# Kernel optimization log

Measured on AMD Instinct MI355X. Metric: run time of the kernel, lower is better.

## Reference

```python
import jax, jax.numpy as jnp
import numpy as np

N_NODES = 50000
IN_DIM = 128
HID = 2 * IN_DIM  # 256, per module: hidden_dim = input_dims * 2
FC1 = 1024
FC2 = 512
N_ACT = 64
N_EDGES = 800000
N_AGENTS = 16384


def _layernorm(h, g, b, eps=1e-5):
    mu = jnp.mean(h, axis=-1, keepdims=True)
    var = jnp.var(h, axis=-1, keepdims=True)
    return (h - mu) * jax.lax.rsqrt(var + eps) * g + b


def setup_inputs() -> dict:
    key = jax.random.key(0)
    ks = jax.random.split(key, 16)
    def u(k, shape, fan_in):
        s = 1.0 / np.sqrt(fan_in)
        return jax.random.uniform(k, shape, jnp.float32, -s, s)
    inp = {}
    inp["x"] = jax.random.normal(ks[0], (N_NODES, IN_DIM), jnp.float32)
    inp["action"] = jax.random.normal(ks[1], (N_AGENTS, N_ACT), jnp.float32)
    inp["edge_index"] = jax.random.randint(ks[2], (2, N_EDGES), 0, N_NODES, jnp.int32)
    inp["agent_idx"] = jax.random.randint(ks[3], (N_AGENTS,), 0, N_NODES, jnp.int32)
    # GCNConv params (linear no bias + separate bias)
    inp["W_gcn"] = u(ks[4], (IN_DIM, HID), IN_DIM)
    inp["b_gcn"] = jnp.zeros((HID,), jnp.float32)
    # fc1, fc2 (custom uniform init per module)
    inp["W1"] = u(ks[5], (HID, FC1), FC1)
    inp["b1"] = u(ks[6], (FC1,), FC1)
    inp["g1"] = jnp.ones((FC1,), jnp.float32)
    inp["beta1"] = jnp.zeros((FC1,), jnp.float32)
    inp["W2"] = u(ks[7], (FC1, FC2), FC2)
    inp["b2"] = u(ks[8], (FC2,), FC2)
    inp["g2"] = jnp.ones((FC2,), jnp.float32)
    inp["beta2"] = jnp.zeros((FC2,), jnp.float32)
    inp["Wa"] = u(ks[9], (N_ACT, FC2), FC2)
    inp["ba"] = u(ks[10], (FC2,), FC2)
    inp["Wq"] = jax.random.uniform(ks[11], (FC2, 1), jnp.float32, -0.003, 0.003)
    inp["bq"] = jax.random.uniform(ks[12], (1,), jnp.float32, -0.003, 0.003)
    return inp


def reference(x, action, W_gcn, b_gcn, W1, b1, g1, beta1, W2, b2, g2, beta2, Wa, ba, Wq, bq, edge_index, agent_idx):
    N = x.shape[0]
    # GCNConv: add self-loops, symmetric D^-1/2 (A+I) D^-1/2 normalization
    loops = jnp.arange(N, dtype=edge_index.dtype)
    src = jnp.concatenate([edge_index[0], loops])
    dst = jnp.concatenate([edge_index[1], loops])
    h = x @ W_gcn  # [N, HID] transform before aggregation
    deg = jax.ops.segment_sum(jnp.ones_like(dst, dtype=h.dtype), dst, num_segments=N)
    dinv = jax.lax.rsqrt(jnp.maximum(deg, 1.0))  # deg >= 1 due to self-loops
    norm = dinv[src] * dinv[dst]  # [E+N]
    agg = jax.ops.segment_sum(h[src] * norm[:, None], dst, num_segments=N) + b_gcn
    # masked gather of agent nodes, then critic MLP
    z = jax.nn.relu(agg[agent_idx])  # [A, HID]
    s = jax.nn.relu(_layernorm(z @ W1 + b1, g1, beta1))
    s = _layernorm(s @ W2 + b2, g2, beta2)
    a = action @ Wa + ba
    sa = jax.nn.relu(s + a)
    return sa @ Wq + bq  # [A, 1]
```

## Files before the change

kernel.cpp:

```cpp
#include <hip/hip_runtime.h>
#include <hip/hip_bf16.h>

typedef _Float16 f16;
typedef _Float16 __attribute__((ext_vector_type(8))) half8;
typedef _Float16 __attribute__((ext_vector_type(4))) half4;
typedef float __attribute__((ext_vector_type(4))) floatx4;

#define IN_DIM 128
#define HID    256
#define FC1    1024
#define FC2    512
#define NACT   64

__device__ __forceinline__ void transpose_tile(const float* __restrict__ in, f16* __restrict__ out,
                                               int K, int N, int bx, int by, int tid) {
    __shared__ f16 tile[32][33];
    int k0 = bx * 32, n0 = by * 32;
    int tx = tid & 31, ty = tid >> 5;
    #pragma unroll
    for (int i = 0; i < 4; ++i)
        tile[ty + i * 8][tx] = (f16)in[(size_t)(k0 + ty + i * 8) * N + n0 + tx];
    __syncthreads();
    #pragma unroll
    for (int i = 0; i < 4; ++i)
        out[(size_t)(n0 + ty + i * 8) * K + k0 + tx] = tile[tx][ty + i * 8];
}

__device__ __forceinline__ void cvt8(const float* __restrict__ in, f16* __restrict__ out, long gi) {
    float4 a = *(const float4*)&in[gi * 8];
    float4 b = *(const float4*)&in[gi * 8 + 4];
    half8 pk;
    pk[0] = (f16)a.x; pk[1] = (f16)a.y; pk[2] = (f16)a.z; pk[3] = (f16)a.w;
    pk[4] = (f16)b.x; pk[5] = (f16)b.y; pk[6] = (f16)b.z; pk[7] = (f16)b.w;
    *(half8*)&out[gi * 8] = pk;
}

__global__ __launch_bounds__(256)
void prep_kernel(const float* __restrict__ Wgcn, const float* __restrict__ W1,
                 const float* __restrict__ W2, const float* __restrict__ Wa,
                 const float* __restrict__ action, const float* __restrict__ x,
                 f16* WgcnT, f16* W1T, f16* W2T, f16* WaT, f16* act16, f16* x16,
                 int* degcnt, int* needed, int* n_needed, int N, int A) {
    int b = blockIdx.x, tid = threadIdx.x;
    if (b < 196) {
        int i = b * 256 + tid;
        if (i < N) { degcnt[i] = 0; needed[i] = 0; }
        if (b == 0 && tid == 0) *n_needed = 0;
        return;
    }
    b -= 196;
    if (b < 32)  { transpose_tile(Wgcn, WgcnT, IN_DIM, HID, b & 3, b >> 2, tid); return; }
    b -= 32;
    if (b < 256) { transpose_tile(W1, W1T, HID, FC1, b & 7, b >> 3, tid); return; }
    b -= 256;
    if (b < 512) { transpose_tile(W2, W2T, FC1, FC2, b & 31, b >> 5, tid); return; }
    b -= 512;
    if (b < 32)  { transpose_tile(Wa, WaT, NACT, FC2, b & 1, b >> 1, tid); return; }
    b -= 32;
    if (b < 512) { cvt8(action, act16, (long)b * 256 + tid); return; }
    b -= 512;
    cvt8(x, x16, (long)b * 256 + tid);
}

__global__ void markdeg_kernel(const int* __restrict__ agent_idx, const int* __restrict__ edst,
                               int* __restrict__ needed, int* __restrict__ needed_list,
                               int* __restrict__ n_needed, int* __restrict__ degcnt, int A, int E) {
    int b = blockIdx.x;
    if (b < 64) {
        int i = b * 256 + threadIdx.x;
        if (i < A) {
            int idx = agent_idx[i];
            if (atomicCAS(&needed[idx], 0, -1) == 0) {
                int p = atomicAdd(n_needed, 1);
                needed_list[p] = idx;
                needed[idx] = p + 1;
            }
        }
        return;
    }
    int e = (b - 64) * 256 + threadIdx.x;
    if (e < E) atomicAdd(&degcnt[edst[e]], 1);
}

__global__ void dss_kernel(const int* __restrict__ degcnt, const int* __restrict__ needed,
                           const int* __restrict__ agent_idx, float* __restrict__ dinv,
                           int* __restrict__ offs, int* __restrict__ partials,
                           int* __restrict__ agent_slot, int N, int A) {
    int b = blockIdx.x;
    if (b < 196) {
        __shared__ int sh[256];
        int tid = threadIdx.x;
        int i = b * 256 + tid;
        int dc = (i < N) ? degcnt[i] : 0;
        if (i < N) dinv[i] = rsqrtf((float)dc + 1.0f);
        int v = (i < N && needed[i] != 0) ? dc : 0;
        sh[tid] = v;
        __syncthreads();
        #pragma unroll
        for (int d = 1; d < 256; d <<= 1) {
            int t = (tid >= d) ? sh[tid - d] : 0;
            __syncthreads();
            sh[tid] += t;
            __syncthreads();
        }
        if (i < N) offs[i] = sh[tid] - v;
        if (tid == 255) partials[b] = sh[255];
        return;
    }
    int i = (b - 196) * 256 + threadIdx.x;
    if (i < A) agent_slot[i] = needed[agent_idx[i]] - 1;
}

__global__ void addback_kernel(int* __restrict__ offs, const int* __restrict__ partials,
                               int* __restrict__ cursor, int n, int nblk) {
    __shared__ int sh[256];
    int tid = threadIdx.x;
    int v = (tid < nblk) ? partials[tid] : 0;
    sh[tid] = v;
    __syncthreads();
    #pragma unroll
    for (int d = 1; d < 256; d <<= 1) {
        int t = (tid >= d) ? sh[tid - d] : 0;
        __syncthreads();
        sh[tid] += t;
        __syncthreads();
    }
    int base = (blockIdx.x == 0) ? 0 : sh[blockIdx.x - 1];
    int i = blockIdx.x * 256 + tid;
    if (i < n) {
        int o = offs[i] + base;
        offs[i] = o;
        cursor[i] = o;
    }
}

__global__ void fill_kernel(const int* __restrict__ src, const int* __restrict__ dst,
                            const int* __restrict__ needed, int* __restrict__ cursor,
                            int* __restrict__ srcbuf, int E) {
    int e = blockIdx.x * blockDim.x + threadIdx.x;
    if (e < E) {
        int d = dst[e];
        if (needed[d] != 0) {
            int pos = atomicAdd(&cursor[d], 1);
            srcbuf[pos] = src[e];
        }
    }
}

__global__ __launch_bounds__(256)
void gather_x_kernel(const int* __restrict__ needed_list, const int* __restrict__ n_needed,
                     const int* __restrict__ offs, const int* __restrict__ degcnt,
                     const int* __restrict__ srcbuf, const float* __restrict__ dinv,
                     const f16* __restrict__ x16, f16* __restrict__ xagg) {
    int w = (blockIdx.x * 256 + threadIdx.x) >> 6;
    int lane = threadIdx.x & 63;
    if (w >= *n_needed) return;
    int d = needed_list[w];
    float dd = dinv[d];
    int beg = offs[d], cnt = degcnt[d];
    union { unsigned u; f16 h[2]; } ld0, ld1, ld2, ld3;
    ld0.u = *(const unsigned*)&x16[(size_t)d * IN_DIM + lane * 2];
    float ax = (float)ld0.h[0] * dd * dd, ay = (float)ld0.h[1] * dd * dd;
    int j = 0;
    for (; j + 3 < cnt; j += 4) {
        int s0 = srcbuf[beg + j], s1 = srcbuf[beg + j + 1];
        int s2 = srcbuf[beg + j + 2], s3 = srcbuf[beg + j + 3];
        float n0 = dinv[s0] * dd, n1 = dinv[s1] * dd;
        float n2 = dinv[s2] * dd, n3 = dinv[s3] * dd;
        ld0.u = *(const unsigned*)&x16[(size_t)s0 * IN_DIM + lane * 2];
        ld1.u = *(const unsigned*)&x16[(size_t)s1 * IN_DIM + lane * 2];
        ld2.u = *(const unsigned*)&x16[(size_t)s2 * IN_DIM + lane * 2];
        ld3.u = *(const unsigned*)&x16[(size_t)s3 * IN_DIM + lane * 2];
        ax = fmaf((float)ld0.h[0], n0, ax); ay = fmaf((float)ld0.h[1], n0, ay);
        ax = fmaf((float)ld1.h[0], n1, ax); ay = fmaf((float)ld1.h[1], n1, ay);
        ax = fmaf((float)ld2.h[0], n2, ax); ay = fmaf((float)ld2.h[1], n2, ay);
        ax = fmaf((float)ld3.h[0], n3, ax); ay = fmaf((float)ld3.h[1], n3, ay);
    }
    for (; j < cnt; ++j) {
        int s0 = srcbuf[beg + j];
        float n0 = dinv[s0] * dd;
        ld0.u = *(const unsigned*)&x16[(size_t)s0 * IN_DIM + lane * 2];
        ax = fmaf((float)ld0.h[0], n0, ax);
        ay = fmaf((float)ld0.h[1], n0, ay);
    }
    union { f16 h[2]; unsigned u; } pk;
    pk.h[0] = (f16)ax; pk.h[1] = (f16)ay;
    *(unsigned*)&xagg[(size_t)w * IN_DIM + lane * 2] = pk.u;
}

__device__ __forceinline__ void swz_decode(int bid, int log2ny, int& bx, int& by) {
    int xcd = bid & 7;
    int pos = bid >> 3;
    bx = (pos >> log2ny) * 8 + xcd;
    by = pos & ((1 << log2ny) - 1);
}

template<bool RELU, bool LIMIT>
__device__ __forceinline__ void gemm_tile(f16* __restrict__ smA, f16* __restrict__ smB,
                                          const f16* __restrict__ A, const f16* __restrict__ BT,
                                          f16* __restrict__ C, const float* __restrict__ bias,
                                          const int* __restrict__ limit,
                                          int bx, int by, int N, int K) {
    if (LIMIT && bx * 64 >= *limit) return;
    const int tid = threadIdx.x;
    const int lane = tid & 63;
    const int wave = tid >> 6;
    const int wr = wave >> 1, wc = wave & 1;
    const long bm = (long)bx * 64, bn = (long)by * 64;

    size_t aoff[2], boff[2];
    #pragma unroll
    for (int t = 0; t < 2; ++t) {
        int ci = t * 256 + tid;
        int r = ci >> 3, s = ci & 7, ks = s ^ (r & 7);
        aoff[t] = (size_t)(bm + r) * K + ks * 8;
        boff[t] = (size_t)(bn + r) * K + ks * 8;
    }
    int aidx[2][2], bidx[2][2];
    const int kc = lane >> 4;
    #pragma unroll
    for (int kk = 0; kk < 2; ++kk) {
        #pragma unroll
        for (int i = 0; i < 2; ++i) {
            int ar = wr * 32 + i * 16 + (lane & 15);
            aidx[kk][i] = ar * 64 + ((kk * 4 + kc) ^ (ar & 7)) * 8;
            int br = wc * 32 + i * 16 + (lane & 15);
            bidx[kk][i] = br * 64 + ((kk * 4 + kc) ^ (br & 7)) * 8;
        }
    }

    const int NT = K >> 6;
    auto stage = [&](int buf, int k0) {
        #pragma unroll
        for (int t = 0; t < 2; ++t) {
            __builtin_amdgcn_global_load_lds(
                (const __attribute__((address_space(1))) void*)(A + aoff[t] + k0),
                (__attribute__((address_space(3))) void*)(&smA[buf * 4096 + (t * 256 + tid) * 8]), 16, 0, 0);
            __builtin_amdgcn_global_load_lds(
                (const __attribute__((address_space(1))) void*)(BT + boff[t] + k0),
                (__attribute__((address_space(3))) void*)(&smB[buf * 4096 + (t * 256 + tid) * 8]), 16, 0, 0);
        }
    };

    floatx4 acc[2][2] = {};
    stage(0, 0);
    asm volatile("s_waitcnt vmcnt(0)" ::: "memory");
    __builtin_amdgcn_s_barrier();
    int cur = 0;
    for (int t = 0; t < NT; ++t) {
        if (t + 1 < NT) stage(cur ^ 1, (t + 1) << 6);
        #pragma unroll
        for (int kk = 0; kk < 2; ++kk) {
            half8 af[2], bf[2];
            #pragma unroll
            for (int i = 0; i < 2; ++i) {
                af[i] = *(const half8*)&smA[cur * 4096 + aidx[kk][i]];
                bf[i] = *(const half8*)&smB[cur * 4096 + bidx[kk][i]];
            }
            #pragma unroll
            for (int mi = 0; mi < 2; ++mi)
                #pragma unroll
                for (int ni = 0; ni < 2; ++ni)
                    acc[mi][ni] = __builtin_amdgcn_mfma_f32_16x16x32_f16(af[mi], bf[ni], acc[mi][ni], 0, 0, 0);
        }
        asm volatile("s_waitcnt vmcnt(0)" ::: "memory");
        __builtin_amdgcn_s_barrier();
        cur ^= 1;
    }
    const int col0 = (int)bn + wc * 32 + (lane & 15);
    const int row0 = (int)bm + wr * 32 + (lane >> 4) * 4;
    #pragma unroll
    for (int ni = 0; ni < 2; ++ni) {
        int col = col0 + ni * 16;
        float bz = bias[col];
        #pragma unroll
        for (int mi = 0; mi < 2; ++mi) {
            #pragma unroll
            for (int q = 0; q < 4; ++q) {
                int row = row0 + mi * 16 + q;
                float v = acc[mi][ni][q] + bz;
                if (RELU) v = fmaxf(v, 0.f);
                C[(size_t)row * N + col] = (f16)v;
            }
        }
    }
}

template<bool RELU, bool LIMIT>
__global__ __launch_bounds__(256)
void gemm_f16_kernel(const f16* __restrict__ A, const f16* __restrict__ BT,
                     f16* __restrict__ C, const float* __restrict__ bias,
                     const int* __restrict__ limit, int N, int K, int log2ny) {
    __shared__ __align__(16) f16 smA[2 * 4096];
    __shared__ __align__(16) f16 smB[2 * 4096];
    int bx, by;
    swz_decode(blockIdx.x, log2ny, bx, by);
    gemm_tile<RELU, LIMIT>(smA, smB, A, BT, C, bias, limit, bx, by, N, K);
}

__global__ __launch_bounds__(256)
void gemm_dual_kernel(const f16* __restrict__ A0, const f16* __restrict__ BT0, f16* __restrict__ C0,
                      const float* __restrict__ bias0, const int* __restrict__ limit, int K0,
                      const f16* __restrict__ A1, const f16* __restrict__ BT1, f16* __restrict__ C1,
                      const float* __restrict__ bias1, int K1, int half, int N) {
    __shared__ __align__(16) f16 smA[2 * 4096];
    __shared__ __align__(16) f16 smB[2 * 4096];
    int bid = blockIdx.x;
    int bx, by;
    if (bid < half) {
        swz_decode(bid, 3, bx, by);
        gemm_tile<false, true>(smA, smB, A0, BT0, C0, bias0, limit, bx, by, N, K0);
    } else {
        swz_decode(bid - half, 3, bx, by);
        gemm_tile<false, false>(smA, smB, A1, BT1, C1, bias1, nullptr, bx, by, N, K1);
    }
}

__global__ __launch_bounds__(256)
void ln_relu_f16_kernel(f16* __restrict__ s, const float* __restrict__ g,
                        const float* __restrict__ b, const int* __restrict__ nn) {
    int row = blockIdx.x;
    if (row >= *nn) return;
    f16* p = s + (size_t)row * FC1;
    int tid = threadIdx.x;
    half4 v = *(const half4*)&p[tid * 4];
    float f0 = (float)v[0], f1 = (float)v[1], f2 = (float)v[2], f3 = (float)v[3];
    float sum = f0 + f1 + f2 + f3;
    float sq = f0 * f0 + f1 * f1 + f2 * f2 + f3 * f3;
    #pragma unroll
    for (int off = 32; off > 0; off >>= 1) {
        sum += __shfl_down(sum, off);
        sq  += __shfl_down(sq, off);
    }
    __shared__ float ssum[4], ssq[4];
    int wid = tid >> 6;
    if ((tid & 63) == 0) { ssum[wid] = sum; ssq[wid] = sq; }
    __syncthreads();
    float tot = ssum[0] + ssum[1] + ssum[2] + ssum[3];
    float tq  = ssq[0] + ssq[1] + ssq[2] + ssq[3];
    float mu = tot * (1.0f / FC1);
    float var = tq * (1.0f / FC1) - mu * mu;
    float rs = rsqrtf(var + 1e-5f);
    float4 gg = *(const float4*)&g[tid * 4];
    float4 bb = *(const float4*)&b[tid * 4];
    half4 o;
    o[0] = (f16)fmaxf((f0 - mu) * rs * gg.x + bb.x, 0.f);
    o[1] = (f16)fmaxf((f1 - mu) * rs * gg.y + bb.y, 0.f);
    o[2] = (f16)fmaxf((f2 - mu) * rs * gg.z + bb.z, 0.f);
    o[3] = (f16)fmaxf((f3 - mu) * rs * gg.w + bb.w, 0.f);
    *(half4*)&p[tid * 4] = o;
}

__global__ __launch_bounds__(256)
void final_f16_kernel(const f16* __restrict__ s2, const f16* __restrict__ ab,
                      const int* __restrict__ agent_slot,
                      const float* __restrict__ g2, const float* __restrict__ b2,
                      const float* __restrict__ Wq, const float* __restrict__ bq,
                      float* __restrict__ out) {
    int row = blockIdx.x;
    int slot = agent_slot[row];
    const f16* p = s2 + (size_t)slot * FC2;
    int tid = threadIdx.x;
    float v0 = (float)p[tid * 2], v1 = (float)p[tid * 2 + 1];
    float sum = v0 + v1;
    float sq = v0 * v0 + v1 * v1;
    #pragma unroll
    for (int off = 32; off > 0; off >>= 1) {
        sum += __shfl_down(sum, off);
        sq  += __shfl_down(sq, off);
    }
    __shared__ float ssum[4], ssq[4], spart[4];
    int wid = tid >> 6;
    if ((tid & 63) == 0) { ssum[wid] = sum; ssq[wid] = sq; }
    __syncthreads();
    float tot = ssum[0] + ssum[1] + ssum[2] + ssum[3];
    float tq  = ssq[0] + ssq[1] + ssq[2] + ssq[3];
    float mu = tot * (1.0f / FC2);
    float var = tq * (1.0f / FC2) - mu * mu;
    float rs = rsqrtf(var + 1e-5f);
    float a0 = (float)ab[(size_t)row * FC2 + tid * 2];
    float a1 = (float)ab[(size_t)row * FC2 + tid * 2 + 1];
    float g0 = g2[tid * 2], g1 = g2[tid * 2 + 1];
    float bb0 = b2[tid * 2], bb1 = b2[tid * 2 + 1];
    float sa0 = fmaxf((v0 - mu) * rs * g0 + bb0 + a0, 0.f);
    float sa1 = fmaxf((v1 - mu) * rs * g1 + bb1 + a1, 0.f);
    float part = sa0 * Wq[tid * 2] + sa1 * Wq[tid * 2 + 1];
    #pragma unroll
    for (int off = 32; off > 0; off >>= 1) part += __shfl_down(part, off);
    if ((tid & 63) == 0) spart[wid] = part;
    __syncthreads();
    if (tid == 0) out[row] = spart[0] + spart[1] + spart[2] + spart[3] + bq[0];
}

extern "C" void kernel_launch(void* const* d_in, const int* in_sizes, int n_in,
                              void* d_out, int out_size, void* d_ws, size_t ws_size,
                              hipStream_t stream) {
    const float* x        = (const float*)d_in[0];
    const float* action   = (const float*)d_in[1];
    const int*   edge     = (const int*)d_in[2];
    const int*   agent_idx= (const int*)d_in[3];
    const float* W_gcn    = (const float*)d_in[4];
    const float* b_gcn    = (const float*)d_in[5];
    const float* W1       = (const float*)d_in[6];
    const float* b1       = (const float*)d_in[7];
    const float* g1       = (const float*)d_in[8];
    const float* beta1    = (const float*)d_in[9];
    const float* W2       = (const float*)d_in[10];
    const float* b2       = (const float*)d_in[11];
    const float* g2       = (const float*)d_in[12];
    const float* beta2    = (const float*)d_in[13];
    const float* Wa       = (const float*)d_in[14];
    const float* ba       = (const float*)d_in[15];
    const float* Wq       = (const float*)d_in[16];
    const float* bq       = (const float*)d_in[17];
    float* out = (float*)d_out;

    const int N = in_sizes[0] / IN_DIM;
    const int E = in_sizes[2] / 2;
    const int A = in_sizes[3];
    const int* esrc = edge;
    const int* edst = edge + E;

    char* ws = (char*)d_ws;
    size_t off = 0;
    auto carve = [&](size_t bytes) -> char* {
        char* p = ws + off;
        off += (bytes + 255) & ~(size_t)255;
        return p;
    };
    int*   degcnt     = (int*)  carve((size_t)N * 4);
    int*   needed     = (int*)  carve((size_t)N * 4);
    float* dinv       = (float*)carve((size_t)N * 4);
    int*   offs       = (int*)  carve((size_t)N * 4);
    int*   cursor     = (int*)  carve((size_t)N * 4);
    int*   partials   = (int*)  carve(1024 * 4);
    int*   needed_list= (int*)  carve((size_t)A * 4);
    int*   n_needed   = (int*)  carve(256);
    int*   agent_slot = (int*)  carve((size_t)A * 4);
    int*   srcbuf     = (int*)  carve((size_t)E * 4);
    f16*   WgcnT      = (f16*)  carve((size_t)HID * IN_DIM * 2);
    f16*   W1T        = (f16*)  carve((size_t)FC1 * HID * 2);
    f16*   W2T        = (f16*)  carve((size_t)FC2 * FC1 * 2);
    f16*   WaT        = (f16*)  carve((size_t)FC2 * NACT * 2);
    f16*   act16      = (f16*)  carve((size_t)A * NACT * 2);
    f16*   x16        = (f16*)  carve((size_t)N * IN_DIM * 2);
    f16*   xagg       = (f16*)  carve((size_t)A * IN_DIM * 2);
    f16*   z          = (f16*)  carve((size_t)A * HID * 2);
    f16*   s1         = (f16*)  carve((size_t)A * FC1 * 2);
    f16*   s2         = (f16*)  carve((size_t)A * FC2 * 2);
    f16*   abuf       = (f16*)  carve((size_t)A * FC2 * 2);
    (void)ws_size;

    const int nblk_scan = (N + 255) / 256;
    const int eblk = (E + 255) / 256;

    prep_kernel<<<196 + 32 + 256 + 512 + 32 + 512 + eblk, 256, 0, stream>>>(
        W_gcn, W1, W2, Wa, action, x, WgcnT, W1T, W2T, WaT, act16, x16,
        degcnt, needed, n_needed, N, A);
    markdeg_kernel<<<64 + eblk, 256, 0, stream>>>(agent_idx, edst, needed, needed_list,
                                                  n_needed, degcnt, A, E);
    dss_kernel<<<nblk_scan + 64, 256, 0, stream>>>(degcnt, needed, agent_idx, dinv,
                                                   offs, partials, agent_slot, N, A);
    addback_kernel<<<nblk_scan, 256, 0, stream>>>(offs, partials, cursor, N, nblk_scan);
    fill_kernel<<<eblk, 256, 0, stream>>>(esrc, edst, needed, cursor, srcbuf, E);
    gather_x_kernel<<<(A + 3) / 4, 256, 0, stream>>>(needed_list, n_needed, offs, degcnt,
                                                     srcbuf, dinv, x16, xagg);
    gemm_f16_kernel<true, true><<<(A / 64) * (HID / 64), 256, 0, stream>>>(
        xagg, WgcnT, z, b_gcn, n_needed, HID, IN_DIM, 2);
    gemm_f16_kernel<false, true><<<(A / 64) * (FC1 / 64), 256, 0, stream>>>(
        z, W1T, s1, b1, n_needed, FC1, HID, 4);
    ln_relu_f16_kernel<<<A, 256, 0, stream>>>(s1, g1, beta1, n_needed);
    gemm_dual_kernel<<<2 * (A / 64) * (FC2 / 64), 256, 0, stream>>>(
        s1, W2T, s2, b2, n_needed, FC1,
        act16, WaT, abuf, ba, NACT, (A / 64) * (FC2 / 64), FC2);
    final_f16_kernel<<<A, 256, 0, stream>>>(s2, abuf, agent_slot, g2, beta2, Wq, bq, out);
}
```

Measured before the change: 168.9 us.

## Add 128x128 MFMA GEMM tile for fc1 and fc2/action GEMMs

Introduces a 128x128 block-tile GEMM variant: each wave computes a 64x64 sub-tile with 4x4 MFMA accumulators, with double-buffered direct global-to-LDS loads. The fc1 GEMM and the dual fc2/action GEMM switch to it, with grid sizes and swizzle widths adjusted to match. The aim is more operand reuse per LDS load and fewer redundant global reads. The cost is fewer blocks, which may leave CUs idle on the smaller grids, along with 64KB of LDS per block and higher register pressure.

```diff
diff --git a/kernel.cpp b/kernel.cpp
--- a/kernel.cpp
+++ b/kernel.cpp
@@ -196,11 +196,11 @@
 }
 
 template<bool RELU, bool LIMIT>
-__device__ __forceinline__ void gemm_tile(f16* __restrict__ smA, f16* __restrict__ smB,
-                                          const f16* __restrict__ A, const f16* __restrict__ BT,
-                                          f16* __restrict__ C, const float* __restrict__ bias,
-                                          const int* __restrict__ limit,
-                                          int bx, int by, int N, int K) {
+__device__ __forceinline__ void gemm_tile64(f16* __restrict__ smA, f16* __restrict__ smB,
+                                            const f16* __restrict__ A, const f16* __restrict__ BT,
+                                            f16* __restrict__ C, const float* __restrict__ bias,
+                                            const int* __restrict__ limit,
+                                            int bx, int by, int N, int K) {
     if (LIMIT && bx * 64 >= *limit) return;
     const int tid = threadIdx.x;
     const int lane = tid & 63;
@@ -288,14 +288,115 @@
 
 template<bool RELU, bool LIMIT>
 __global__ __launch_bounds__(256)
-void gemm_f16_kernel(const f16* __restrict__ A, const f16* __restrict__ BT,
-                     f16* __restrict__ C, const float* __restrict__ bias,
-                     const int* __restrict__ limit, int N, int K, int log2ny) {
+void gemm64_kernel(const f16* __restrict__ A, const f16* __restrict__ BT,
+                   f16* __restrict__ C, const float* __restrict__ bias,
+                   const int* __restrict__ limit, int N, int K, int log2ny) {
     __shared__ __align__(16) f16 smA[2 * 4096];
     __shared__ __align__(16) f16 smB[2 * 4096];
     int bx, by;
     swz_decode(blockIdx.x, log2ny, bx, by);
-    gemm_tile<RELU, LIMIT>(smA, smB, A, BT, C, bias, limit, bx, by, N, K);
+    gemm_tile64<RELU, LIMIT>(smA, smB, A, BT, C, bias, limit, bx, by, N, K);
+}
+
+template<bool LIMIT>
+__device__ __forceinline__ void gemm_tile128(f16* __restrict__ smA, f16* __restrict__ smB,
+                                             const f16* __restrict__ A, const f16* __restrict__ BT,
+                                             f16* __restrict__ C, const float* __restrict__ bias,
+                                             const int* __restrict__ limit,
+                                             int bx, int by, int N, int K) {
+    if (LIMIT && bx * 128 >= *limit) return;
+    const int tid = threadIdx.x;
+    const int lane = tid & 63;
+    const int wave = tid >> 6;
+    const int wr = wave >> 1, wc = wave & 1;
+    const long bm = (long)bx * 128, bn = (long)by * 128;
+
+    size_t aoff[4], boff[4];
+    #pragma unroll
+    for (int t = 0; t < 4; ++t) {
+        int ci = t * 256 + tid;
+        int r = ci >> 3, s = ci & 7, ks = s ^ (r & 7);
+        aoff[t] = (size_t)(bm + r) * K + ks * 8;
+        boff[t] = (size_t)(bn + r) * K + ks * 8;
+    }
+    int aidx[2][4], bidx[2][4];
+    const int kc = lane >> 4;
+    #pragma unroll
+    for (int kk = 0; kk < 2; ++kk) {
+        #pragma unroll
+        for (int i = 0; i < 4; ++i) {
+            int ar = wr * 64 + i * 16 + (lane & 15);
+            aidx[kk][i] = ar * 64 + ((kk * 4 + kc) ^ (ar & 7)) * 8;
+            int br = wc * 64 + i * 16 + (lane & 15);
+            bidx[kk][i] = br * 64 + ((kk * 4 + kc) ^ (br & 7)) * 8;
+        }
+    }
+
+    const int NT = K >> 6;
+    auto stage = [&](int buf, int k0) {
+        #pragma unroll
+        for (int t = 0; t < 4; ++t) {
+            __builtin_amdgcn_global_load_lds(
+                (const __attribute__((address_space(1))) void*)(A + aoff[t] + k0),
+                (__attribute__((address_space(3))) void*)(&smA[buf * 8192 + (t * 256 + tid) * 8]), 16, 0, 0);
+            __builtin_amdgcn_global_load_lds(
+                (const __attribute__((address_space(1))) void*)(BT + boff[t] + k0),
+                (__attribute__((address_space(3))) void*)(&smB[buf * 8192 + (t * 256 + tid) * 8]), 16, 0, 0);
+        }
+    };
+
+    floatx4 acc[4][4] = {};
+    stage(0, 0);
+    asm volatile("s_waitcnt vmcnt(0)" ::: "memory");
+    __builtin_amdgcn_s_barrier();
+    int cur = 0;
+    for (int t = 0; t < NT; ++t) {
+        if (t + 1 < NT) stage(cur ^ 1, (t + 1) << 6);
+        #pragma unroll
+        for (int kk = 0; kk < 2; ++kk) {
+            half8 af[4], bf[4];
+            #pragma unroll
+            for (int i = 0; i < 4; ++i) {
+                af[i] = *(const half8*)&smA[cur * 8192 + aidx[kk][i]];
+                bf[i] = *(const half8*)&smB[cur * 8192 + bidx[kk][i]];
+            }
+            #pragma unroll
+            for (int mi = 0; mi < 4; ++mi)
+                #pragma unroll
+                for (int ni = 0; ni < 4; ++ni)
+                    acc[mi][ni] = __builtin_amdgcn_mfma_f32_16x16x32_f16(af[mi], bf[ni], acc[mi][ni], 0, 0, 0);
+        }
+        asm volatile("s_waitcnt vmcnt(0)" ::: "memory");
+        __builtin_amdgcn_s_barrier();
+        cur ^= 1;
+    }
+    const int col0 = (int)bn + wc * 64 + (lane & 15);
+    const int row0 = (int)bm + wr * 64 + (lane >> 4) * 4;
+    #pragma unroll
+    for (int ni = 0; ni < 4; ++ni) {
+        int col = col0 + ni * 16;
+        float bz = bias[col];
+        #pragma unroll
+        for (int mi = 0; mi < 4; ++mi) {
+            #pragma unroll
+            for (int q = 0; q < 4; ++q) {
+                int row = row0 + mi * 16 + q;
+                C[(size_t)row * N + col] = (f16)(acc[mi][ni][q] + bz);
+            }
+        }
+    }
+}
+
+template<bool LIMIT>
+__global__ __launch_bounds__(256)
+void gemm128_kernel(const f16* __restrict__ A, const f16* __restrict__ BT,
+                    f16* __restrict__ C, const float* __restrict__ bias,
+                    const int* __restrict__ limit, int N, int K, int log2ny) {
+    __shared__ __align__(16) f16 smA[2 * 8192];
+    __shared__ __align__(16) f16 smB[2 * 8192];
+    int bx, by;
+    swz_decode(blockIdx.x, log2ny, bx, by);
+    gemm_tile128<LIMIT>(smA, smB, A, BT, C, bias, limit, bx, by, N, K);
 }
 
 __global__ __launch_bounds__(256)
@@ -303,16 +404,16 @@
                       const float* __restrict__ bias0, const int* __restrict__ limit, int K0,
                       const f16* __restrict__ A1, const f16* __restrict__ BT1, f16* __restrict__ C1,
                       const float* __restrict__ bias1, int K1, int half, int N) {
-    __shared__ __align__(16) f16 smA[2 * 4096];
-    __shared__ __align__(16) f16 smB[2 * 4096];
+    __shared__ __align__(16) f16 smA[2 * 8192];
+    __shared__ __align__(16) f16 smB[2 * 8192];
     int bid = blockIdx.x;
     int bx, by;
     if (bid < half) {
-        swz_decode(bid, 3, bx, by);
-        gemm_tile<false, true>(smA, smB, A0, BT0, C0, bias0, limit, bx, by, N, K0);
+        swz_decode(bid, 2, bx, by);
+        gemm_tile128<true>(smA, smB, A0, BT0, C0, bias0, limit, bx, by, N, K0);
     } else {
-        swz_decode(bid - half, 3, bx, by);
-        gemm_tile<false, false>(smA, smB, A1, BT1, C1, bias1, nullptr, bx, by, N, K1);
+        swz_decode(bid - half, 2, bx, by);
+        gemm_tile128<false>(smA, smB, A1, BT1, C1, bias1, nullptr, bx, by, N, K1);
     }
 }
 
@@ -465,13 +566,13 @@
     fill_kernel<<<eblk, 256, 0, stream>>>(esrc, edst, needed, cursor, srcbuf, E);
     gather_x_kernel<<<(A + 3) / 4, 256, 0, stream>>>(needed_list, n_needed, offs, degcnt,
                                                      srcbuf, dinv, x16, xagg);
-    gemm_f16_kernel<true, true><<<(A / 64) * (HID / 64), 256, 0, stream>>>(
+    gemm64_kernel<true, true><<<(A / 64) * (HID / 64), 256, 0, stream>>>(
         xagg, WgcnT, z, b_gcn, n_needed, HID, IN_DIM, 2);
-    gemm_f16_kernel<false, true><<<(A / 64) * (FC1 / 64), 256, 0, stream>>>(
-        z, W1T, s1, b1, n_needed, FC1, HID, 4);
+    gemm128_kernel<true><<<(A / 128) * (FC1 / 128), 256, 0, stream>>>(
+        z, W1T, s1, b1, n_needed, FC1, HID, 3);
     ln_relu_f16_kernel<<<A, 256, 0, stream>>>(s1, g1, beta1, n_needed);
-    gemm_dual_kernel<<<2 * (A / 64) * (FC2 / 64), 256, 0, stream>>>(
+    gemm_dual_kernel<<<2 * (A / 128) * (FC2 / 128), 256, 0, stream>>>(
         s1, W2T, s2, b2, n_needed, FC1,
-        act16, WaT, abuf, ba, NACT, (A / 64) * (FC2 / 64), FC2);
+        act16, WaT, abuf, ba, NACT, (A / 128) * (FC2 / 128), FC2);
     final_f16_kernel<<<A, 256, 0, stream>>>(s2, abuf, agent_slot, g2, beta2, Wq, bq, out);
 }
```

Result: faster. 164.8 us (-2.4%).
